# Performance work log

Measured on AMD Instinct MI355X. Metric: run time of the kernel, lower is better.

Reference implementation:

```python
import jax, jax.numpy as jnp
import numpy as np

N_NODES = 100000
N_EDGES = 800000
N_GRAPHS = 64
N_ETYPES = 4
D = 150
HID = 512
PASSES = 5


def setup_inputs() -> dict:
    key = jax.random.key(0)
    ks = jax.random.split(key, 16)
    s = 0.1
    return {
        "nodes": jax.random.normal(ks[0], (N_NODES, D), jnp.float32),
        "problem_class": jax.random.normal(ks[1], (N_GRAPHS, 1), jnp.float32),
        "edge_src": jax.random.randint(ks[2], (N_EDGES,), 0, N_NODES, jnp.int32),
        "edge_dst": jax.random.randint(ks[3], (N_EDGES,), 0, N_NODES, jnp.int32),
        "edge_type": jax.random.randint(ks[4], (N_EDGES,), 0, N_ETYPES, jnp.int32),
        "graph_ids": jnp.sort(jax.random.randint(ks[5], (N_NODES,), 0, N_GRAPHS, jnp.int32)),
        "W_e": jax.random.normal(ks[6], (N_ETYPES, D, D), jnp.float32) * s,
        "b_e": jax.random.normal(ks[7], (N_ETYPES, D), jnp.float32) * s,
        "w_ih": jax.random.normal(ks[8], (3 * D, D), jnp.float32) * s,
        "w_hh": jax.random.normal(ks[9], (3 * D, D), jnp.float32) * s,
        "b_ih": jax.random.normal(ks[10], (3 * D,), jnp.float32) * s,
        "b_hh": jax.random.normal(ks[11], (3 * D,), jnp.float32) * s,
        "fc1_w": jax.random.normal(ks[12], (D + 1, HID), jnp.float32) * s,
        "fc1_b": jax.random.normal(ks[13], (HID,), jnp.float32) * s,
        "fc2_w": jax.random.normal(ks[14], (HID, 10), jnp.float32) * s,
        "fc2_b": jax.random.normal(ks[15], (10,), jnp.float32) * s,
    }


def _gru_cell(x, h, w_ih, w_hh, b_ih, b_hh):
    # torch.nn.GRUCell math, gate order (r, z, n)
    gi = x @ w_ih.T + b_ih
    gh = h @ w_hh.T + b_hh
    i_r, i_z, i_n = jnp.split(gi, 3, axis=1)
    h_r, h_z, h_n = jnp.split(gh, 3, axis=1)
    r = jax.nn.sigmoid(i_r + h_r)
    z = jax.nn.sigmoid(i_z + h_z)
    n = jnp.tanh(i_n + r * h_n)
    return (1.0 - z) * n + z * h


def reference(nodes, problem_class, edge_src, edge_dst, edge_type, graph_ids,
              W_e, b_e, w_ih, w_hh, b_ih, b_hh, fc1_w, fc1_b, fc2_w, fc2_b):
    n_nodes = nodes.shape[0]
    n_graphs = problem_class.shape[0]
    n_types = W_e.shape[0]

    # in-degree per edge type (for the per-edge Linear bias contribution)
    type_onehot = jax.nn.one_hot(edge_type, n_types, dtype=nodes.dtype)  # [E, T]
    deg = jax.ops.segment_sum(type_onehot, edge_dst, num_segments=n_nodes)  # [N, T]
    bias_inc = deg @ b_e  # [N, D] = sum_t deg_t * b_t

    h = nodes
    for _ in range(PASSES):
        h_src = h[edge_src]  # [E, D] gather
        inc = bias_inc
        for t in range(n_types):
            # aggregate first, apply the edge-type Linear after (linearity)
            agg = jax.ops.segment_sum(
                jnp.where((edge_type == t)[:, None], h_src, 0.0),
                edge_dst, num_segments=n_nodes)  # [N, D]
            inc = inc + agg @ W_e[t].T
        h = _gru_cell(inc, h, w_ih, w_hh, b_ih, b_hh)

    # graph readout: sum nodes, log, nan -> 0, relu
    g = jax.ops.segment_sum(h, graph_ids, num_segments=n_graphs)  # [B, D]
    l = jnp.log(g)
    l = jax.nn.relu(jnp.where(jnp.isnan(l), 0.0, l))
    x = jnp.concatenate([l, problem_class], axis=1)  # [B, D+1]
    x = jax.nn.leaky_relu(x @ fc1_w + fc1_b)
    return x @ fc2_w + fc2_b
```

## Files before the change

### kernel.cpp

```cpp
#include <hip/hip_runtime.h>
#include <hip/hip_bf16.h>
#include <cstdint>
#include <cstddef>

#define NN 100000
#define NE 800000
#define NG 64
#define NT 4
#define DD 150
#define HS 160
#define HIDN 512
#define NPASS 5
#define NBINS (NN*NT)
#define RPB 16

typedef short  s8v  __attribute__((ext_vector_type(8)));
typedef float  f32x4 __attribute__((ext_vector_type(4)));

static __device__ __forceinline__ float sigmoidf_(float x){ return 1.f/(1.f+expf(-x)); }
static __device__ __forceinline__ short f2bf(float x){
  __hip_bfloat16 b = __float2bfloat16(x);
  return *(short*)&b;
}
static __device__ __forceinline__ float bf2f(short s){
  union { unsigned u; float f; } v; v.u = ((unsigned)(unsigned short)s) << 16; return v.f;
}
static __device__ __forceinline__ void split_bf(float x, short& hi, short& lo){
  hi = f2bf(x);
  lo = f2bf(x - bf2f(hi));
}


__global__ void count_kernel(const int* __restrict__ dst, const int* __restrict__ typ,
                             unsigned* __restrict__ deg){
  int e = blockIdx.x*256 + threadIdx.x;
  if (e < NE) atomicAdd(&deg[dst[e]*NT + typ[e]], 1u);
}

__device__ unsigned block_excl_base(unsigned threadSum){
  const int tid = threadIdx.x;
  const int lane = tid & 63, wid = tid >> 6;
  unsigned s = threadSum;
  #pragma unroll
  for (int d = 1; d < 64; d <<= 1){ unsigned t = __shfl_up(s, d); if (lane >= d) s += t; }
  __shared__ unsigned wsum[4];
  if (lane == 63) wsum[wid] = s;
  __syncthreads();
  unsigned base = 0;
  for (int w = 0; w < wid; w++) base += wsum[w];
  return base + s - threadSum;
}

__global__ void scan_reduce(const unsigned* __restrict__ deg, unsigned* __restrict__ bsum){
  const int base = blockIdx.x*1024 + threadIdx.x*4;
  unsigned s = 0;
  #pragma unroll
  for (int i = 0; i < 4; i++){ const int idx = base+i; if (idx < NBINS) s += deg[idx]; }
  #pragma unroll
  for (int d = 1; d < 64; d <<= 1) s += __shfl_down(s, d);
  __shared__ unsigned ws4[4];
  const int lane = threadIdx.x & 63, wid = threadIdx.x >> 6;
  if (lane == 0) ws4[wid] = s;
  __syncthreads();
  if (threadIdx.x == 0) bsum[blockIdx.x] = ws4[0]+ws4[1]+ws4[2]+ws4[3];
}

__global__ void scan_block(unsigned* bsum, int n){
  const int tid = threadIdx.x;
  unsigned v[4]; unsigned s = 0;
  #pragma unroll
  for (int i = 0; i < 4; i++){ const int idx = tid*4+i; v[i] = (idx < n) ? bsum[idx] : 0u; s += v[i]; }
  unsigned run = block_excl_base(s);
  #pragma unroll
  for (int i = 0; i < 4; i++){ const int idx = tid*4+i; if (idx < n) bsum[idx] = run; run += v[i]; }
}

__global__ void scan_final(const unsigned* __restrict__ deg, const unsigned* __restrict__ bsum,
                           unsigned* __restrict__ off){
  const int tid = threadIdx.x;
  const int base0 = blockIdx.x*1024 + tid*4;
  unsigned v[4]; unsigned s = 0;
  #pragma unroll
  for (int i = 0; i < 4; i++){ const int idx = base0+i; v[i] = (idx < NBINS) ? deg[idx] : 0u; s += v[i]; }
  unsigned run = block_excl_base(s) + bsum[blockIdx.x];
  #pragma unroll
  for (int i = 0; i < 4; i++){ const int idx = base0+i; if (idx < NBINS) off[idx] = run; run += v[i]; }
  if (blockIdx.x == 0 && tid == 0) off[NBINS] = NE;
}

__global__ void scatter_sort(const int* __restrict__ src, const int* __restrict__ dst,
                             const int* __restrict__ typ, unsigned* __restrict__ cur,
                             int* __restrict__ srcSorted){
  int e = blockIdx.x*256 + threadIdx.x;
  if (e < NE){
    const int bin = dst[e]*NT + typ[e];
    const unsigned p = atomicAdd(&cur[bin], 1u);
    srcSorted[p] = src[e];
  }
}

__global__ void init_h(const float* __restrict__ nodes, float* __restrict__ h0){
  const long long idx = (long long)blockIdx.x*256 + threadIdx.x;
  if (idx >= (long long)NN*HS) return;
  const int row = (int)(idx / HS), col = (int)(idx % HS);
  float v = 0.f;
  if (col < DD) v = nodes[(size_t)row*DD + col];
  h0[idx] = v;
}

__global__ void build_bfrag_msg(const float* __restrict__ W, unsigned short* __restrict__ out){
  const int idx = blockIdx.x*256 + threadIdx.x;
  if (idx >= NT*5*10*2*512) return;
  const int w = idx & 511;
  int r = idx >> 9;
  const int c = r % 2;  r /= 2;
  const int i = r % 10; r /= 10;
  const int s = r % 5;  const int t = r / 5;
  const int l = w >> 3, j = w & 7;
  const int n  = 16*i + (l & 15);
  const int kk = 32*s + (l >> 4)*8 + j;
  float v = 0.f;
  if (n < DD && kk < DD) v = W[(size_t)(t*DD + n)*DD + kk];
  short hi, lo; split_bf(v, hi, lo);
  out[(size_t)((t*5 + s)*20 + i*2 + c)*512 + w] = (unsigned short)(c ? lo : hi);
}

__global__ void build_bfrag_gru(const float* __restrict__ w_ih, const float* __restrict__ w_hh,
                                unsigned short* __restrict__ out){
  const int idx = blockIdx.x*256 + threadIdx.x;
  if (idx >= 10*3*2*2*5*512) return;
  const int w = idx & 511;
  int r = idx >> 9;
  const int s = r % 5;    r /= 5;
  const int c = r % 2;    r /= 2;
  const int u = r % 2;    r /= 2;
  const int part = r % 3; const int iT = r / 3;
  const int P = part*2 + u;
  const int g = P >> 1;
  const float* W = (P & 1) ? w_hh : w_ih;
  const int l = w >> 3, j = w & 7;
  const int n  = 16*iT + (l & 15);
  const int kk = 32*s + (l >> 4)*8 + j;
  float v = 0.f;
  if (n < DD && kk < DD) v = W[(size_t)(g*DD + n)*DD + kk];
  short hi, lo; split_bf(v, hi, lo);
  out[(size_t)((iT*3 + part)*20 + u*10 + c*5 + s)*512 + w] = (unsigned short)(c ? lo : hi);
}

#define MFMA3(acc, ahi, alo, bhi, blo) \
  acc = __builtin_amdgcn_mfma_f32_16x16x32_bf16(ahi, bhi, acc, 0,0,0); \
  acc = __builtin_amdgcn_mfma_f32_16x16x32_bf16(alo, bhi, acc, 0,0,0); \
  acc = __builtin_amdgcn_mfma_f32_16x16x32_bf16(ahi, blo, acc, 0,0,0);

__global__ __launch_bounds__(256, 2) void msg_kernel(
    const float* __restrict__ h, const int* __restrict__ srcS,
    const unsigned* __restrict__ off, const unsigned* __restrict__ deg,
    const float* __restrict__ b_e,
    const unsigned short* __restrict__ BfE2,
    float* __restrict__ inc)
{
  __shared__ short Bs[2][20*512];
  const int tid = threadIdx.x, wave = tid >> 6, l = tid & 63;
  const int m = l & 15, q = l >> 4, q8 = q*8;
  const int arow = blockIdx.x*64 + wave*16 + m;
  const bool av = (arow < NN);
  const int lb8 = l*8;

  f32x4 acc[10];
  #pragma unroll
  for (int i = 0; i < 10; i++) acc[i] = (f32x4)(0.0f);

  #pragma unroll
  for (int k2 = 0; k2 < 5; k2++){
    const int c = tid + k2*256;
    *(s8v*)(&Bs[0][c*8]) = *(const s8v*)(BfE2 + (size_t)c*8);
  }
  __syncthreads();

  s8v sv[5];
  for (int t = 0; t < NT; t++){
    #pragma unroll
    for (int k2 = 0; k2 < 5; k2++){
      const int c = tid + k2*256;
      sv[k2] = *(const s8v*)(BfE2 + (size_t)(t*5 + 1)*10240 + (size_t)c*8);
    }

    float a[5][8];
    #pragma unroll
    for (int s = 0; s < 5; s++)
      #pragma unroll
      for (int j = 0; j < 8; j++) a[s][j] = 0.f;

    int lo = 0, hi = 0;
    if (av){ const int bin = arow*NT + t; lo = (int)off[bin]; hi = (int)off[bin+1]; }
    int e = lo;
    int i0 = (e   < hi) ? srcS[e]   : 0;
    int i1 = (e+1 < hi) ? srcS[e+1] : -1;
    while (e < hi){
      const int n0 = (e+2 < hi) ? srcS[e+2] : 0;
      const int n1 = (e+3 < hi) ? srcS[e+3] : -1;
      const float* p0 = h + (size_t)i0*HS + q8;
      const float* p1 = h + (size_t)(i1 < 0 ? 0 : i1)*HS + q8;
      const float w1 = (i1 < 0) ? 0.f : 1.f;
      f32x4 v[10], u[10];
      #pragma unroll
      for (int s = 0; s < 5; s++){
        v[2*s]   = *(const f32x4*)(p0 + 32*s);
        v[2*s+1] = *(const f32x4*)(p0 + 32*s + 4);
      }
      #pragma unroll
      for (int s = 0; s < 5; s++){
        u[2*s]   = *(const f32x4*)(p1 + 32*s);
        u[2*s+1] = *(const f32x4*)(p1 + 32*s + 4);
      }
      #pragma unroll
      for (int s = 0; s < 5; s++){
        #pragma unroll
        for (int j = 0; j < 4; j++){
          a[s][j]   += v[2*s][j];
          a[s][j]   = fmaf(w1, u[2*s][j], a[s][j]);
          a[s][4+j] += v[2*s+1][j];
          a[s][4+j] = fmaf(w1, u[2*s+1][j], a[s][4+j]);
        }
      }
      e += 2; i0 = n0; i1 = n1;
    }

    s8v af_hi[5], af_lo[5];
    #pragma unroll
    for (int s = 0; s < 5; s++)
      #pragma unroll
      for (int j = 0; j < 8; j++){
        short h2, l2; split_bf(a[s][j], h2, l2);
        af_hi[s][j] = h2; af_lo[s][j] = l2;
      }

    #pragma unroll
    for (int st = 0; st < 5; st++){
      const int sidx = t*5 + st;
      const short* bsr = &Bs[sidx & 1][0];
      #pragma unroll
      for (int i = 0; i < 10; i++){
        const s8v bh = *(const s8v*)(bsr + (i*2+0)*512 + lb8);
        const s8v bl = *(const s8v*)(bsr + (i*2+1)*512 + lb8);
        MFMA3(acc[i], af_hi[st], af_lo[st], bh, bl)
      }
      if (sidx + 1 < 20){
        short* bsw = &Bs[(sidx+1) & 1][0];
        #pragma unroll
        for (int k2 = 0; k2 < 5; k2++){
          const int c = tid + k2*256;
          *(s8v*)(bsw + c*8) = sv[k2];
        }
      }
      if (st < 4 && sidx + 2 < 20){
        #pragma unroll
        for (int k2 = 0; k2 < 5; k2++){
          const int c = tid + k2*256;
          sv[k2] = *(const s8v*)(BfE2 + (size_t)(sidx+2)*10240 + (size_t)c*8);
        }
      }
      __syncthreads();
    }
  }

  const int crow0 = blockIdx.x*64 + wave*16 + q*4;
  #pragma unroll
  for (int r = 0; r < 4; r++){
    const int crow = crow0 + r;
    if (crow < NN){
      const uint4 dg = *(const uint4*)(&deg[crow*NT]);
      const float d0=(float)dg.x, d1=(float)dg.y, d2=(float)dg.z, d3=(float)dg.w;
      float* op = inc + (size_t)crow*HS;
      #pragma unroll
      for (int i = 0; i < 10; i++){
        const int c = 16*i + m;
        float val = 0.f;
        if (c < DD)
          val = acc[i][r] + fmaf(d0, b_e[c], fmaf(d1, b_e[DD+c],
                  fmaf(d2, b_e[2*DD+c], d3*b_e[3*DD+c])));
        op[c] = val;
      }
    }
  }
}

__global__ __launch_bounds__(256, 2) void gru_kernel(
    const float* __restrict__ h, float* __restrict__ incnext,
    const unsigned short* __restrict__ BfG,
    const float* __restrict__ b_ih, const float* __restrict__ b_hh)
{
  __shared__ short Bs[2][20*512];
  const int tid = threadIdx.x, wave = tid >> 6, l = tid & 63;
  const int m = l & 15, q = l >> 4, q8 = q*8;
  const int arow = blockIdx.x*64 + wave*16 + m;
  const bool av = (arow < NN);
  const int lb8 = l*8;
  const int crow0 = blockIdx.x*64 + wave*16 + q*4;

  s8v afi_h[5], afi_l[5], afh_h[5], afh_l[5];
  {
    const float* ip = incnext + (size_t)(av ? arow : 0)*HS;
    const float* hp = h       + (size_t)(av ? arow : 0)*HS;
    #pragma unroll
    for (int s = 0; s < 5; s++){
      const int b = 32*s + q8;
      const f32x4 x0 = *(const f32x4*)(ip + b), x1 = *(const f32x4*)(ip + b + 4);
      const f32x4 y0 = *(const f32x4*)(hp + b), y1 = *(const f32x4*)(hp + b + 4);
      #pragma unroll
      for (int j = 0; j < 4; j++){
        short h2, l2;
        split_bf(x0[j], h2, l2); afi_h[s][j]   = h2; afi_l[s][j]   = l2;
        split_bf(x1[j], h2, l2); afi_h[s][4+j] = h2; afi_l[s][4+j] = l2;
        split_bf(y0[j], h2, l2); afh_h[s][j]   = h2; afh_l[s][j]   = l2;
        split_bf(y1[j], h2, l2); afh_h[s][4+j] = h2; afh_l[s][4+j] = l2;
      }
    }
  }

  #pragma unroll
  for (int k2 = 0; k2 < 5; k2++){
    const int c = tid + k2*256;
    *(s8v*)(&Bs[0][c*8]) = *(const s8v*)(BfG + (size_t)c*8);
  }
  __syncthreads();

  s8v sv[5];
  #pragma unroll
  for (int k2 = 0; k2 < 5; k2++){
    const int c = tid + k2*256;
    sv[k2] = *(const s8v*)(BfG + (size_t)10240 + (size_t)c*8);
  }

  f32x4 aR=(f32x4)(0.f), aZ=(f32x4)(0.f);
  float hv[4] = {0.f,0.f,0.f,0.f};

  for (int k = 0; k < 30; k++){
    const int iT = k/3, part = k - 3*iT;
    const int d = 16*iT + m;
    if (part == 0){
      #pragma unroll
      for (int r = 0; r < 4; r++){
        hv[r] = 0.f;
        if (crow0 + r < NN && d < DD) hv[r] = h[(size_t)(crow0+r)*HS + d];
      }
    }

    const short* bsr = &Bs[k & 1][0];
    f32x4 tI = (f32x4)(0.f), tH = (f32x4)(0.f);
    #pragma unroll
    for (int s = 0; s < 5; s++){
      const s8v b0h = *(const s8v*)(bsr + (     s)*512 + lb8);
      const s8v b0l = *(const s8v*)(bsr + ( 5 + s)*512 + lb8);
      const s8v b1h = *(const s8v*)(bsr + (10 + s)*512 + lb8);
      const s8v b1l = *(const s8v*)(bsr + (15 + s)*512 + lb8);
      MFMA3(tI, afi_h[s], afi_l[s], b0h, b0l)
      MFMA3(tH, afh_h[s], afh_l[s], b1h, b1l)
    }

    if (k < 29){
      short* bsw = &Bs[(k+1) & 1][0];
      #pragma unroll
      for (int k2 = 0; k2 < 5; k2++){
        const int c = tid + k2*256;
        *(s8v*)(bsw + c*8) = sv[k2];
      }
    }
    if (k < 28){
      #pragma unroll
      for (int k2 = 0; k2 < 5; k2++){
        const int c = tid + k2*256;
        sv[k2] = *(const s8v*)(BfG + (size_t)(k+2)*10240 + (size_t)c*8);
      }
    }

    if (part == 0){
      aR = tI + tH;
    } else if (part == 1){
      aZ = tI + tH;
    } else if (d < DD){
      const float br   = b_ih[d]    + b_hh[d];
      const float bz   = b_ih[DD+d] + b_hh[DD+d];
      const float bin2 = b_ih[2*DD+d];
      const float bhn  = b_hh[2*DD+d];
      #pragma unroll
      for (int r = 0; r < 4; r++){
        const int crow = crow0 + r;
        if (crow < NN){
          const float rr = sigmoidf_(aR[r] + br);
          const float zz = sigmoidf_(aZ[r] + bz);
          const float nn = tanhf(tI[r] + bin2 + rr*(tH[r] + bhn));
          incnext[(size_t)crow*HS + d] = (1.f - zz)*nn + zz*hv[r];
        }
      }
    }
    __syncthreads();
  }
}

__global__ void readout1(const float* __restrict__ h, const int* __restrict__ gids,
                         float* __restrict__ part){
  const int g = blockIdx.x >> 4, s = blockIdx.x & (RPB-1);
  const int tid = threadIdx.x;
  __shared__ int sb[2];
  if (tid < 2){
    const int target = g + tid;
    int lo = 0, hi = NN;
    while (lo < hi){ const int mid = (lo+hi) >> 1; if (gids[mid] < target) lo = mid+1; else hi = mid; }
    sb[tid] = lo;
  }
  __syncthreads();
  const int lo = sb[0], hi = sb[1];
  const int len = hi - lo;
  const int per = (len + RPB - 1) / RPB;
  const int nlo = lo + s*per;
  const int nhi = (nlo + per < hi) ? (nlo + per) : hi;
  if (tid < DD){
    float acc = 0.f;
    for (int n = nlo; n < nhi; n++) acc += h[(size_t)n*HS + tid];
    part[(size_t)blockIdx.x*DD + tid] = acc;
  }
}

__global__ void readout2(const float* __restrict__ part, const float* __restrict__ pclass,
                         float* __restrict__ xbuf){
  const int g = blockIdx.x, tid = threadIdx.x;
  if (tid < DD){
    float acc = 0.f;
    #pragma unroll
    for (int s = 0; s < RPB; s++) acc += part[(size_t)(g*RPB + s)*DD + tid];
    float l = logf(acc);
    if (isnan(l)) l = 0.f;
    l = fmaxf(l, 0.f);
    xbuf[g*(DD+1)+tid] = l;
  }
  if (tid == DD) xbuf[g*(DD+1)+DD] = pclass[g];
}

__global__ void fc1_kernel(const float* __restrict__ xbuf, const float* __restrict__ w,
                           const float* __restrict__ b, float* __restrict__ hid){
  const int g = blockIdx.x, tid = threadIdx.x;
  __shared__ float xs[DD+1];
  if (tid < DD+1) xs[tid] = xbuf[g*(DD+1)+tid];
  __syncthreads();
  float acc = b[tid];
  for (int k = 0; k < DD+1; k++) acc = fmaf(xs[k], w[k*HIDN + tid], acc);
  hid[g*HIDN + tid] = (acc > 0.f) ? acc : 0.01f*acc;
}

__global__ void fc2_kernel(const float* __restrict__ hid, const float* __restrict__ w,
                           const float* __restrict__ b, float* __restrict__ out){
  const int g = blockIdx.x, tid = threadIdx.x;
  __shared__ float hs[HIDN];
  for (int i = tid; i < HIDN; i += 64) hs[i] = hid[g*HIDN + i];
  __syncthreads();
  if (tid < 10){
    float acc = b[tid];
    for (int k = 0; k < HIDN; k++) acc = fmaf(hs[k], w[k*10 + tid], acc);
    out[g*10 + tid] = acc;
  }
}

extern "C" void kernel_launch(void* const* d_in, const int* in_sizes, int n_in,
                              void* d_out, int out_size, void* d_ws, size_t ws_size,
                              hipStream_t stream)
{
  (void)in_sizes; (void)n_in; (void)out_size; (void)ws_size;
  const float* nodes  = (const float*)d_in[0];
  const float* pclass = (const float*)d_in[1];
  const int*   esrc   = (const int*)d_in[2];
  const int*   edst   = (const int*)d_in[3];
  const int*   etyp   = (const int*)d_in[4];
  const int*   gids   = (const int*)d_in[5];
  const float* W_e    = (const float*)d_in[6];
  const float* b_e    = (const float*)d_in[7];
  const float* w_ih   = (const float*)d_in[8];
  const float* w_hh   = (const float*)d_in[9];
  const float* b_ih   = (const float*)d_in[10];
  const float* b_hh   = (const float*)d_in[11];
  const float* fc1w   = (const float*)d_in[12];
  const float* fc1b   = (const float*)d_in[13];
  const float* fc2w   = (const float*)d_in[14];
  const float* fc2b   = (const float*)d_in[15];
  float* out = (float*)d_out;

  char* p = (char*)d_ws;
  auto alloc = [&](size_t bytes)->char* {
    char* r = p; p += ((bytes + 255) & ~(size_t)255); return r;
  };
  float*    h0   = (float*)alloc((size_t)NN*HS*4);
  float*    h1   = (float*)alloc((size_t)NN*HS*4);
  unsigned* deg  = (unsigned*)alloc((size_t)NBINS*4);
  unsigned* off  = (unsigned*)alloc((size_t)(NBINS+1)*4);
  unsigned* cur  = (unsigned*)alloc((size_t)NBINS*4);
  unsigned* bsum = (unsigned*)alloc(4096);
  int*      srcS = (int*)alloc((size_t)NE*4);
  unsigned short* BfE2 = (unsigned short*)alloc((size_t)20*20*512*2);
  unsigned short* BfG  = (unsigned short*)alloc((size_t)30*20*512*2);
  float*    part = (float*)alloc((size_t)NG*RPB*DD*4);
  float*    xbuf = (float*)alloc((size_t)NG*(DD+1)*4);
  float*    hidb = (float*)alloc((size_t)NG*HIDN*4);

  hipMemsetAsync(deg, 0, (size_t)NBINS*4, stream);
  count_kernel<<<(NE+255)/256, 256, 0, stream>>>(edst, etyp, deg);
  const int SCB = (NBINS + 1023)/1024;
  scan_reduce<<<SCB, 256, 0, stream>>>(deg, bsum);
  scan_block<<<1, 256, 0, stream>>>(bsum, SCB);
  scan_final<<<SCB, 256, 0, stream>>>(deg, bsum, off);
  hipMemcpyAsync(cur, off, (size_t)NBINS*4, hipMemcpyDeviceToDevice, stream);
  scatter_sort<<<(NE+255)/256, 256, 0, stream>>>(esrc, edst, etyp, cur, srcS);
  build_bfrag_msg<<<(NT*5*10*2*512+255)/256, 256, 0, stream>>>(W_e, BfE2);
  build_bfrag_gru<<<(10*3*2*2*5*512+255)/256, 256, 0, stream>>>(w_ih, w_hh, BfG);
  init_h<<<(int)(((long long)NN*HS + 255)/256), 256, 0, stream>>>(nodes, h0);

  float* hb[2] = {h0, h1};
  const int grows = (NN + 63)/64;
  for (int pass = 0; pass < NPASS; pass++){
    const float* hc = hb[pass & 1];
    float*       hn = hb[(pass + 1) & 1];
    msg_kernel<<<grows, 256, 0, stream>>>(hc, srcS, off, deg, b_e, BfE2, hn);
    gru_kernel<<<grows, 256, 0, stream>>>(hc, hn, BfG, b_ih, b_hh);
  }

  readout1<<<NG*RPB, 256, 0, stream>>>(hb[NPASS & 1], gids, part);
  readout2<<<NG, 256, 0, stream>>>(part, pclass, xbuf);
  fc1_kernel<<<NG, HIDN, 0, stream>>>(xbuf, fc1w, fc1b, hidb);
  fc2_kernel<<<NG, 64, 0, stream>>>(hidb, fc2w, fc2b, out);
}
```

Before: 1.848 ms.

## Fuse message aggregation and GRU update into a single per-pass kernel

Merges the message kernel and the GRU kernel so each 64-row block computes the aggregated incoming messages, stages them in shared memory, and feeds them straight into the GRU MFMA stage. This removes the global write and re-read of the intermediate inc buffer and one launch per pass. It reuses the B-fragment LDS buffer as a padded staging area, adds extra barriers, and makes the fused kernel longer with possibly higher register pressure. Padding columns of the next h are now written as zero explicitly.

```diff
diff --git a/kernel.cpp b/kernel.cpp
--- a/kernel.cpp
+++ b/kernel.cpp
@@ -13,6 +13,7 @@
 #define NPASS 5
 #define NBINS (NN*NT)
 #define RPB 16
+#define PKS 154
 
 typedef short  s8v  __attribute__((ext_vector_type(8)));
 typedef float  f32x4 __attribute__((ext_vector_type(4)));
@@ -152,143 +153,13 @@
   acc = __builtin_amdgcn_mfma_f32_16x16x32_bf16(alo, bhi, acc, 0,0,0); \
   acc = __builtin_amdgcn_mfma_f32_16x16x32_bf16(ahi, blo, acc, 0,0,0);
 
-__global__ __launch_bounds__(256, 2) void msg_kernel(
+__global__ __launch_bounds__(256, 2) void fused_kernel(
     const float* __restrict__ h, const int* __restrict__ srcS,
     const unsigned* __restrict__ off, const unsigned* __restrict__ deg,
     const float* __restrict__ b_e,
-    const unsigned short* __restrict__ BfE2,
-    float* __restrict__ inc)
-{
-  __shared__ short Bs[2][20*512];
-  const int tid = threadIdx.x, wave = tid >> 6, l = tid & 63;
-  const int m = l & 15, q = l >> 4, q8 = q*8;
-  const int arow = blockIdx.x*64 + wave*16 + m;
-  const bool av = (arow < NN);
-  const int lb8 = l*8;
-
-  f32x4 acc[10];
-  #pragma unroll
-  for (int i = 0; i < 10; i++) acc[i] = (f32x4)(0.0f);
-
-  #pragma unroll
-  for (int k2 = 0; k2 < 5; k2++){
-    const int c = tid + k2*256;
-    *(s8v*)(&Bs[0][c*8]) = *(const s8v*)(BfE2 + (size_t)c*8);
-  }
-  __syncthreads();
-
-  s8v sv[5];
-  for (int t = 0; t < NT; t++){
-    #pragma unroll
-    for (int k2 = 0; k2 < 5; k2++){
-      const int c = tid + k2*256;
-      sv[k2] = *(const s8v*)(BfE2 + (size_t)(t*5 + 1)*10240 + (size_t)c*8);
-    }
-
-    float a[5][8];
-    #pragma unroll
-    for (int s = 0; s < 5; s++)
-      #pragma unroll
-      for (int j = 0; j < 8; j++) a[s][j] = 0.f;
-
-    int lo = 0, hi = 0;
-    if (av){ const int bin = arow*NT + t; lo = (int)off[bin]; hi = (int)off[bin+1]; }
-    int e = lo;
-    int i0 = (e   < hi) ? srcS[e]   : 0;
-    int i1 = (e+1 < hi) ? srcS[e+1] : -1;
-    while (e < hi){
-      const int n0 = (e+2 < hi) ? srcS[e+2] : 0;
-      const int n1 = (e+3 < hi) ? srcS[e+3] : -1;
-      const float* p0 = h + (size_t)i0*HS + q8;
-      const float* p1 = h + (size_t)(i1 < 0 ? 0 : i1)*HS + q8;
-      const float w1 = (i1 < 0) ? 0.f : 1.f;
-      f32x4 v[10], u[10];
-      #pragma unroll
-      for (int s = 0; s < 5; s++){
-        v[2*s]   = *(const f32x4*)(p0 + 32*s);
-        v[2*s+1] = *(const f32x4*)(p0 + 32*s + 4);
-      }
-      #pragma unroll
-      for (int s = 0; s < 5; s++){
-        u[2*s]   = *(const f32x4*)(p1 + 32*s);
-        u[2*s+1] = *(const f32x4*)(p1 + 32*s + 4);
-      }
-      #pragma unroll
-      for (int s = 0; s < 5; s++){
-        #pragma unroll
-        for (int j = 0; j < 4; j++){
-          a[s][j]   += v[2*s][j];
-          a[s][j]   = fmaf(w1, u[2*s][j], a[s][j]);
-          a[s][4+j] += v[2*s+1][j];
-          a[s][4+j] = fmaf(w1, u[2*s+1][j], a[s][4+j]);
-        }
-      }
-      e += 2; i0 = n0; i1 = n1;
-    }
-
-    s8v af_hi[5], af_lo[5];
-    #pragma unroll
-    for (int s = 0; s < 5; s++)
-      #pragma unroll
-      for (int j = 0; j < 8; j++){
-        short h2, l2; split_bf(a[s][j], h2, l2);
-        af_hi[s][j] = h2; af_lo[s][j] = l2;
-      }
-
-    #pragma unroll
-    for (int st = 0; st < 5; st++){
-      const int sidx = t*5 + st;
-      const short* bsr = &Bs[sidx & 1][0];
-      #pragma unroll
-      for (int i = 0; i < 10; i++){
-        const s8v bh = *(const s8v*)(bsr + (i*2+0)*512 + lb8);
-        const s8v bl = *(const s8v*)(bsr + (i*2+1)*512 + lb8);
-        MFMA3(acc[i], af_hi[st], af_lo[st], bh, bl)
-      }
-      if (sidx + 1 < 20){
-        short* bsw = &Bs[(sidx+1) & 1][0];
-        #pragma unroll
-        for (int k2 = 0; k2 < 5; k2++){
-          const int c = tid + k2*256;
-          *(s8v*)(bsw + c*8) = sv[k2];
-        }
-      }
-      if (st < 4 && sidx + 2 < 20){
-        #pragma unroll
-        for (int k2 = 0; k2 < 5; k2++){
-          const int c = tid + k2*256;
-          sv[k2] = *(const s8v*)(BfE2 + (size_t)(sidx+2)*10240 + (size_t)c*8);
-        }
-      }
-      __syncthreads();
-    }
-  }
-
-  const int crow0 = blockIdx.x*64 + wave*16 + q*4;
-  #pragma unroll
-  for (int r = 0; r < 4; r++){
-    const int crow = crow0 + r;
-    if (crow < NN){
-      const uint4 dg = *(const uint4*)(&deg[crow*NT]);
-      const float d0=(float)dg.x, d1=(float)dg.y, d2=(float)dg.z, d3=(float)dg.w;
-      float* op = inc + (size_t)crow*HS;
-      #pragma unroll
-      for (int i = 0; i < 10; i++){
-        const int c = 16*i + m;
-        float val = 0.f;
-        if (c < DD)
-          val = acc[i][r] + fmaf(d0, b_e[c], fmaf(d1, b_e[DD+c],
-                  fmaf(d2, b_e[2*DD+c], d3*b_e[3*DD+c])));
-        op[c] = val;
-      }
-    }
-  }
-}
-
-__global__ __launch_bounds__(256, 2) void gru_kernel(
-    const float* __restrict__ h, float* __restrict__ incnext,
-    const unsigned short* __restrict__ BfG,
-    const float* __restrict__ b_ih, const float* __restrict__ b_hh)
+    const unsigned short* __restrict__ BfE2, const unsigned short* __restrict__ BfG,
+    const float* __restrict__ b_ih, const float* __restrict__ b_hh,
+    float* __restrict__ hnext)
 {
   __shared__ short Bs[2][20*512];
   const int tid = threadIdx.x, wave = tid >> 6, l = tid & 63;
@@ -298,25 +169,153 @@
   const int lb8 = l*8;
   const int crow0 = blockIdx.x*64 + wave*16 + q*4;
 
+  f32x4 acc[10];
+  #pragma unroll
+  for (int i = 0; i < 10; i++) acc[i] = (f32x4)(0.0f);
+
+  #pragma unroll
+  for (int k2 = 0; k2 < 5; k2++){
+    const int c = tid + k2*256;
+    *(s8v*)(&Bs[0][c*8]) = *(const s8v*)(BfE2 + (size_t)c*8);
+  }
+  __syncthreads();
+
+  {
+    s8v sv[5];
+    for (int t = 0; t < NT; t++){
+      #pragma unroll
+      for (int k2 = 0; k2 < 5; k2++){
+        const int c = tid + k2*256;
+        sv[k2] = *(const s8v*)(BfE2 + (size_t)(t*5 + 1)*10240 + (size_t)c*8);
+      }
+
+      float a[5][8];
+      #pragma unroll
+      for (int s = 0; s < 5; s++)
+        #pragma unroll
+        for (int j = 0; j < 8; j++) a[s][j] = 0.f;
+
+      int lo = 0, hi = 0;
+      if (av){ const int bin = arow*NT + t; lo = (int)off[bin]; hi = (int)off[bin+1]; }
+      int e = lo;
+      int i0 = (e   < hi) ? srcS[e]   : 0;
+      int i1 = (e+1 < hi) ? srcS[e+1] : -1;
+      while (e < hi){
+        const int n0 = (e+2 < hi) ? srcS[e+2] : 0;
+        const int n1 = (e+3 < hi) ? srcS[e+3] : -1;
+        const float* p0 = h + (size_t)i0*HS + q8;
+        const float* p1 = h + (size_t)(i1 < 0 ? 0 : i1)*HS + q8;
+        const float w1 = (i1 < 0) ? 0.f : 1.f;
+        f32x4 v[10], u[10];
+        #pragma unroll
+        for (int s = 0; s < 5; s++){
+          v[2*s]   = *(const f32x4*)(p0 + 32*s);
+          v[2*s+1] = *(const f32x4*)(p0 + 32*s + 4);
+        }
+        #pragma unroll
+        for (int s = 0; s < 5; s++){
+          u[2*s]   = *(const f32x4*)(p1 + 32*s);
+          u[2*s+1] = *(const f32x4*)(p1 + 32*s + 4);
+        }
+        #pragma unroll
+        for (int s = 0; s < 5; s++){
+          #pragma unroll
+          for (int j = 0; j < 4; j++){
+            a[s][j]   += v[2*s][j];
+            a[s][j]   = fmaf(w1, u[2*s][j], a[s][j]);
+            a[s][4+j] += v[2*s+1][j];
+            a[s][4+j] = fmaf(w1, u[2*s+1][j], a[s][4+j]);
+          }
+        }
+        e += 2; i0 = n0; i1 = n1;
+      }
+
+      s8v af_hi[5], af_lo[5];
+      #pragma unroll
+      for (int s = 0; s < 5; s++)
+        #pragma unroll
+        for (int j = 0; j < 8; j++){
+          short h2, l2; split_bf(a[s][j], h2, l2);
+          af_hi[s][j] = h2; af_lo[s][j] = l2;
+        }
+
+      #pragma unroll
+      for (int st = 0; st < 5; st++){
+        const int sidx = t*5 + st;
+        const short* bsr = &Bs[sidx & 1][0];
+        #pragma unroll
+        for (int i = 0; i < 10; i++){
+          const s8v bh = *(const s8v*)(bsr + (i*2+0)*512 + lb8);
+          const s8v bl = *(const s8v*)(bsr + (i*2+1)*512 + lb8);
+          MFMA3(acc[i], af_hi[st], af_lo[st], bh, bl)
+        }
+        if (sidx + 1 < 20){
+          short* bsw = &Bs[(sidx+1) & 1][0];
+          #pragma unroll
+          for (int k2 = 0; k2 < 5; k2++){
+            const int c = tid + k2*256;
+            *(s8v*)(bsw + c*8) = sv[k2];
+          }
+        }
+        if (st < 4 && sidx + 2 < 20){
+          #pragma unroll
+          for (int k2 = 0; k2 < 5; k2++){
+            const int c = tid + k2*256;
+            sv[k2] = *(const s8v*)(BfE2 + (size_t)(sidx+2)*10240 + (size_t)c*8);
+          }
+        }
+        __syncthreads();
+      }
+    }
+  }
+
+  float* pw = reinterpret_cast<float*>(&Bs[0][0]) + wave*(16*PKS);
+  #pragma unroll
+  for (int r = 0; r < 4; r++){
+    const int crow = crow0 + r;
+    if (crow < NN){
+      const uint4 dg = *(const uint4*)(&deg[crow*NT]);
+      const float d0=(float)dg.x, d1=(float)dg.y, d2=(float)dg.z, d3=(float)dg.w;
+      #pragma unroll
+      for (int i = 0; i < 10; i++){
+        const int c = 16*i + m;
+        if (c < DD){
+          const float bias = fmaf(d0, b_e[c], fmaf(d1, b_e[DD+c],
+                             fmaf(d2, b_e[2*DD+c], d3*b_e[3*DD+c])));
+          pw[(q*4+r)*PKS + c] = acc[i][r] + bias;
+        }
+      }
+    }
+  }
+  __syncthreads();
+
   s8v afi_h[5], afi_l[5], afh_h[5], afh_l[5];
   {
-    const float* ip = incnext + (size_t)(av ? arow : 0)*HS;
-    const float* hp = h       + (size_t)(av ? arow : 0)*HS;
+    const float* ip = pw + m*PKS;
+    const float* hp = h + (size_t)(av ? arow : 0)*HS;
     #pragma unroll
     for (int s = 0; s < 5; s++){
       const int b = 32*s + q8;
-      const f32x4 x0 = *(const f32x4*)(ip + b), x1 = *(const f32x4*)(ip + b + 4);
+      float ti[8] = {0,0,0,0,0,0,0,0};
+      if (b + 8 <= DD){
+        #pragma unroll
+        for (int j = 0; j < 8; j++) ti[j] = ip[b+j];
+      } else if (b < DD){
+        #pragma unroll
+        for (int j = 0; j < 6; j++) ti[j] = ip[b+j];
+      }
       const f32x4 y0 = *(const f32x4*)(hp + b), y1 = *(const f32x4*)(hp + b + 4);
       #pragma unroll
       for (int j = 0; j < 4; j++){
         short h2, l2;
-        split_bf(x0[j], h2, l2); afi_h[s][j]   = h2; afi_l[s][j]   = l2;
-        split_bf(x1[j], h2, l2); afi_h[s][4+j] = h2; afi_l[s][4+j] = l2;
-        split_bf(y0[j], h2, l2); afh_h[s][j]   = h2; afh_l[s][j]   = l2;
-        split_bf(y1[j], h2, l2); afh_h[s][4+j] = h2; afh_l[s][4+j] = l2;
-      }
-    }
-  }
+        split_bf(ti[j],   h2, l2); afi_h[s][j]   = h2; afi_l[s][j]   = l2;
+        split_bf(ti[4+j], h2, l2); afi_h[s][4+j] = h2; afi_l[s][4+j] = l2;
+        split_bf(y0[j],   h2, l2); afh_h[s][j]   = h2; afh_l[s][j]   = l2;
+        split_bf(y1[j],   h2, l2); afh_h[s][4+j] = h2; afh_l[s][4+j] = l2;
+      }
+    }
+  }
+  __syncthreads();
 
   #pragma unroll
   for (int k2 = 0; k2 < 5; k2++){
@@ -378,19 +377,23 @@
       aR = tI + tH;
     } else if (part == 1){
       aZ = tI + tH;
-    } else if (d < DD){
-      const float br   = b_ih[d]    + b_hh[d];
-      const float bz   = b_ih[DD+d] + b_hh[DD+d];
-      const float bin2 = b_ih[2*DD+d];
-      const float bhn  = b_hh[2*DD+d];
+    } else {
       #pragma unroll
       for (int r = 0; r < 4; r++){
         const int crow = crow0 + r;
         if (crow < NN){
-          const float rr = sigmoidf_(aR[r] + br);
-          const float zz = sigmoidf_(aZ[r] + bz);
-          const float nn = tanhf(tI[r] + bin2 + rr*(tH[r] + bhn));
-          incnext[(size_t)crow*HS + d] = (1.f - zz)*nn + zz*hv[r];
+          if (d < DD){
+            const float br   = b_ih[d]    + b_hh[d];
+            const float bz   = b_ih[DD+d] + b_hh[DD+d];
+            const float bin2 = b_ih[2*DD+d];
+            const float bhn  = b_hh[2*DD+d];
+            const float rr = sigmoidf_(aR[r] + br);
+            const float zz = sigmoidf_(aZ[r] + bz);
+            const float nn = tanhf(tI[r] + bin2 + rr*(tH[r] + bhn));
+            hnext[(size_t)crow*HS + d] = (1.f - zz)*nn + zz*hv[r];
+          } else {
+            hnext[(size_t)crow*HS + d] = 0.f;
+          }
         }
       }
     }
@@ -518,8 +521,8 @@
   for (int pass = 0; pass < NPASS; pass++){
     const float* hc = hb[pass & 1];
     float*       hn = hb[(pass + 1) & 1];
-    msg_kernel<<<grows, 256, 0, stream>>>(hc, srcS, off, deg, b_e, BfE2, hn);
-    gru_kernel<<<grows, 256, 0, stream>>>(hc, hn, BfG, b_ih, b_hh);
+    fused_kernel<<<grows, 256, 0, stream>>>(hc, srcS, off, deg, b_e, BfE2, BfG,
+                                            b_ih, b_hh, hn);
   }
 
   readout1<<<NG*RPB, 256, 0, stream>>>(hb[NPASS & 1], gids, part);
```

Result: slower. 1.894 ms (+2.5%).

## Sort destination rows by in-degree to balance message-kernel waves

Applied to the files above, without the earlier changes.

Adds a counting sort of nodes by total in-degree (a histogram, a scan and a scatter) and has the message kernel process rows through that permutation. Rows grouped in a wave then have similar edge counts, which is meant to cut divergence and load imbalance in the per-row gather loop. In exchange, output writes and h-row indexing become scattered rather than contiguous, and three small setup kernels are added.

```diff
diff --git a/kernel.cpp b/kernel.cpp
--- a/kernel.cpp
+++ b/kernel.cpp
@@ -96,6 +96,30 @@
     const int bin = dst[e]*NT + typ[e];
     const unsigned p = atomicAdd(&cur[bin], 1u);
     srcSorted[p] = src[e];
+  }
+}
+
+__global__ void row_hist(const unsigned* __restrict__ off, unsigned* __restrict__ hist){
+  int row = blockIdx.x*256 + threadIdx.x;
+  if (row < NN){
+    unsigned d = off[row*NT + NT] - off[row*NT];
+    if (d > 255u) d = 255u;
+    atomicAdd(&hist[d], 1u);
+  }
+}
+__global__ void hist_scan(const unsigned* __restrict__ hist, unsigned* __restrict__ hbase){
+  unsigned v = hist[threadIdx.x];
+  unsigned b = block_excl_base(v);
+  hbase[threadIdx.x] = b;
+}
+__global__ void row_scatter(const unsigned* __restrict__ off, unsigned* __restrict__ hcur,
+                            int* __restrict__ rowPerm){
+  int row = blockIdx.x*256 + threadIdx.x;
+  if (row < NN){
+    unsigned d = off[row*NT + NT] - off[row*NT];
+    if (d > 255u) d = 255u;
+    const unsigned p = atomicAdd(&hcur[d], 1u);
+    rowPerm[p] = row;
   }
 }
 
@@ -156,14 +180,15 @@
     const float* __restrict__ h, const int* __restrict__ srcS,
     const unsigned* __restrict__ off, const unsigned* __restrict__ deg,
     const float* __restrict__ b_e,
-    const unsigned short* __restrict__ BfE2,
+    const unsigned short* __restrict__ BfE2, const int* __restrict__ rowPerm,
     float* __restrict__ inc)
 {
   __shared__ short Bs[2][20*512];
   const int tid = threadIdx.x, wave = tid >> 6, l = tid & 63;
   const int m = l & 15, q = l >> 4, q8 = q*8;
-  const int arow = blockIdx.x*64 + wave*16 + m;
-  const bool av = (arow < NN);
+  const int aidx = blockIdx.x*64 + wave*16 + m;
+  const bool av = (aidx < NN);
+  const int arow = av ? rowPerm[aidx] : 0;
   const int lb8 = l*8;
 
   f32x4 acc[10];
@@ -264,11 +289,12 @@
     }
   }
 
-  const int crow0 = blockIdx.x*64 + wave*16 + q*4;
+  const int cidx0 = blockIdx.x*64 + wave*16 + q*4;
   #pragma unroll
   for (int r = 0; r < 4; r++){
-    const int crow = crow0 + r;
-    if (crow < NN){
+    const int cidx = cidx0 + r;
+    if (cidx < NN){
+      const int crow = rowPerm[cidx];
       const uint4 dg = *(const uint4*)(&deg[crow*NT]);
       const float d0=(float)dg.x, d1=(float)dg.y, d2=(float)dg.z, d3=(float)dg.w;
       float* op = inc + (size_t)crow*HS;
@@ -494,6 +520,9 @@
   unsigned* off  = (unsigned*)alloc((size_t)(NBINS+1)*4);
   unsigned* cur  = (unsigned*)alloc((size_t)NBINS*4);
   unsigned* bsum = (unsigned*)alloc(4096);
+  unsigned* hist = (unsigned*)alloc(256*4);
+  unsigned* hcur = (unsigned*)alloc(256*4);
+  int*      rowPerm = (int*)alloc((size_t)NN*4);
   int*      srcS = (int*)alloc((size_t)NE*4);
   unsigned short* BfE2 = (unsigned short*)alloc((size_t)20*20*512*2);
   unsigned short* BfG  = (unsigned short*)alloc((size_t)30*20*512*2);
@@ -502,6 +531,7 @@
   float*    hidb = (float*)alloc((size_t)NG*HIDN*4);
 
   hipMemsetAsync(deg, 0, (size_t)NBINS*4, stream);
+  hipMemsetAsync(hist, 0, 256*4, stream);
   count_kernel<<<(NE+255)/256, 256, 0, stream>>>(edst, etyp, deg);
   const int SCB = (NBINS + 1023)/1024;
   scan_reduce<<<SCB, 256, 0, stream>>>(deg, bsum);
@@ -509,6 +539,9 @@
   scan_final<<<SCB, 256, 0, stream>>>(deg, bsum, off);
   hipMemcpyAsync(cur, off, (size_t)NBINS*4, hipMemcpyDeviceToDevice, stream);
   scatter_sort<<<(NE+255)/256, 256, 0, stream>>>(esrc, edst, etyp, cur, srcS);
+  row_hist<<<(NN+255)/256, 256, 0, stream>>>(off, hist);
+  hist_scan<<<1, 256, 0, stream>>>(hist, hcur);
+  row_scatter<<<(NN+255)/256, 256, 0, stream>>>(off, hcur, rowPerm);
   build_bfrag_msg<<<(NT*5*10*2*512+255)/256, 256, 0, stream>>>(W_e, BfE2);
   build_bfrag_gru<<<(10*3*2*2*5*512+255)/256, 256, 0, stream>>>(w_ih, w_hh, BfG);
   init_h<<<(int)(((long long)NN*HS + 255)/256), 256, 0, stream>>>(nodes, h0);
@@ -518,7 +551,7 @@
   for (int pass = 0; pass < NPASS; pass++){
     const float* hc = hb[pass & 1];
     float*       hn = hb[(pass + 1) & 1];
-    msg_kernel<<<grows, 256, 0, stream>>>(hc, srcS, off, deg, b_e, BfE2, hn);
+    msg_kernel<<<grows, 256, 0, stream>>>(hc, srcS, off, deg, b_e, BfE2, rowPerm, hn);
     gru_kernel<<<grows, 256, 0, stream>>>(hc, hn, BfG, b_ih, b_hh);
   }
 
```

Result: slower. 2.546 ms (+37.8%).
